# Optimization experiments

Hardware: AMD Instinct MI355X
Metric: run time of the kernel (lower is better)

Reference implementation:

```python
import jax, jax.numpy as jnp
import numpy as np

EPS = 1e-5
K = 3  # involution kernel size


def bin_act(x):
    # STE binary activation: forward = sign(x), backward via piecewise poly
    m1 = (x < -1).astype(jnp.float32)
    m2 = (x < 0).astype(jnp.float32)
    m3 = (x < 1).astype(jnp.float32)
    out = -1.0 * m1 + (x * x + 2 * x) * (1 - m1)
    out = out * m2 + (-x * x + 2 * x) * (1 - m2)
    out = out * m3 + 1.0 * (1 - m3)
    sg = jax.lax.stop_gradient
    return sg(jnp.sign(x)) - sg(out) + out


def bin_conv1x1(x, w):
    # BinaryConv with kernel_size=1: w is (O, I, 1, 1)
    sf = jnp.mean(jnp.abs(w), axis=(1, 2, 3), keepdims=True)
    bw = sf * jnp.sign(w)
    rw = jnp.clip(w, -1.0, 1.0)
    sg = jax.lax.stop_gradient
    f = sg(bw) - sg(rw) + rw  # (O, I, 1, 1)
    return jnp.einsum('oi,bihw->bohw', f[:, :, 0, 0], x)


def batchnorm(x, gamma, beta):
    # training-mode BN over (N, H, W) per channel, biased variance
    m = jnp.mean(x, axis=(0, 2, 3), keepdims=True)
    v = jnp.mean((x - m) ** 2, axis=(0, 2, 3), keepdims=True)
    xn = (x - m) * jax.lax.rsqrt(v + EPS)
    return gamma.reshape(1, -1, 1, 1) * xn + beta.reshape(1, -1, 1, 1)


def prelu(x, a):
    return jnp.maximum(x, 0) + a.reshape(1, -1, 1, 1) * jnp.minimum(x, 0)


def setup_inputs() -> dict:
    key = jax.random.key(0)
    ks = jax.random.split(key, 8)
    B, C, H, W = 8, 64, 128, 128
    Cr = C // 2           # reduce_rate = 2
    KK = K * K            # group = 1
    inp = {
        'x': jax.random.normal(ks[0], (B, C, H, W), dtype=jnp.float32),
        'pre_bias_b': jnp.zeros((1, C, 1, 1), jnp.float32),
        'pre_conv_w': jax.random.uniform(ks[1], (C, C, 1, 1), jnp.float32) * 0.001,
        'pre_gamma': jnp.ones((C,), jnp.float32),
        'pre_beta': jnp.zeros((C,), jnp.float32),
        'pre_a': jnp.full((C,), 0.25, jnp.float32),
        'mid_bias_b': jnp.zeros((1, C, 1, 1), jnp.float32),
        'reduce_w': jax.random.uniform(ks[2], (Cr, C, 1, 1), jnp.float32) * 0.001,
        'span_w': jax.random.uniform(ks[3], (KK, Cr, 1, 1), jnp.float32) * 0.001,
        'mid_gamma': jnp.ones((C,), jnp.float32),
        'mid_beta': jnp.zeros((C,), jnp.float32),
        'mid_a': jnp.full((C,), 0.25, jnp.float32),
        'post_bias_b': jnp.zeros((1, C, 1, 1), jnp.float32),
        'post_conv_w': jax.random.uniform(ks[4], (C, C, 1, 1), jnp.float32) * 0.001,
        'post_gamma': jnp.ones((C,), jnp.float32),
        'post_beta': jnp.zeros((C,), jnp.float32),
    }
    return inp


def reference(x, pre_bias_b, pre_conv_w, pre_gamma, pre_beta, pre_a,
              mid_bias_b, reduce_w, span_w, mid_gamma, mid_beta, mid_a,
              post_bias_b, post_conv_w, post_gamma, post_beta):
    B, C, H, W = x.shape
    h = bin_act(x)
    h = h + pre_bias_b
    h = bin_conv1x1(h, pre_conv_w)
    h = batchnorm(h, pre_gamma, pre_beta)
    h = prelu(h, pre_a)
    h = h + mid_bias_b
    # kernel branch (AvgPool2d(1,1) is identity for stride=1)
    ker = bin_conv1x1(bin_conv1x1(h, reduce_w), span_w)  # (B, K*K, H, W)
    # unfold: 3x3 patches, pad=1, stride=1 -> (B, C, K*K, H, W)
    hp = jnp.pad(h, ((0, 0), (0, 0), (1, 1), (1, 1)))
    patches = jnp.stack(
        [hp[:, :, i:i + H, j:j + W] for i in range(K) for j in range(K)],
        axis=2)
    out = jnp.sum(patches * ker[:, None, :, :, :], axis=2)  # (B, C, H, W)
    out = batchnorm(out, mid_gamma, mid_beta)
    out = jax.nn.relu(out)
    out = prelu(out, mid_a)
    out = out + post_bias_b
    out = bin_conv1x1(out, post_conv_w)
    out = batchnorm(out, post_gamma, post_beta)
    return out + x  # downsample is Identity (stride=1)
```

## Files before the change

kernel.cpp:

```cpp
#include <hip/hip_runtime.h>

#define B_   8
#define C_   64
#define HW   16384
#define CHW  (C_*HW)
#define NPIX (B_*HW)
#define EPS_ 1e-5f

typedef unsigned short u16;
typedef unsigned int   u32;
typedef __attribute__((ext_vector_type(8))) short bf16x8;
typedef __attribute__((ext_vector_type(4))) float f32x4;

__device__ __forceinline__ float sgnf(float v){ return (float)((v>0.f)-(v<0.f)); }
__device__ __forceinline__ float bf2f(u16 h){ return __uint_as_float(((u32)h)<<16); }
__device__ __forceinline__ u16 f2bf(float f){
    u32 u = __float_as_uint(f);
    u += 0x7fffu + ((u>>16)&1u);
    return (u16)(u>>16);
}
__device__ __forceinline__ u32 pack2(float a, float b){
    return (u32)f2bf(a) | ((u32)f2bf(b)<<16);
}

__global__ void prep(const float* __restrict__ pre_w, const float* __restrict__ pre_bias,
                     const float* __restrict__ red_w, const float* __restrict__ span_w,
                     const float* __restrict__ post_w,
                     u32* __restrict__ wb, float* __restrict__ AB,
                     float* __restrict__ Wq, float* __restrict__ M){
    __shared__ float sr[32], ss[9];
    int t = threadIdx.x;
    if (t < 64){
        float s = 0.f;
        for (int i = 0; i < 64; i++) s += fabsf(pre_w[t*64+i]);
        float alpha = s * (1.f/64.f);
        u32 b0 = 0, b1 = 0;
        float c0 = 0.f;
        for (int i = 0; i < 32; i++){
            b0 |= (__float_as_uint(pre_w[t*64+i]) >> 31) << i;
            b1 |= (__float_as_uint(pre_w[t*64+32+i]) >> 31) << i;
        }
        for (int i = 0; i < 64; i++)
            c0 += alpha * sgnf(pre_w[t*64+i]) * pre_bias[i];
        wb[2*t]   = b0;
        wb[2*t+1] = b1;
        AB[t]     = -2.f * alpha;
        AB[64+t]  = 64.f * alpha + c0;

        float s2 = 0.f;
        for (int i = 0; i < 64; i++) s2 += fabsf(post_w[t*64+i]);
        s2 *= (1.f/64.f);
        for (int i = 0; i < 64; i++) Wq[t*64+i] = s2 * sgnf(post_w[t*64+i]);
    }
    if (t < 32){
        float s = 0.f;
        for (int i = 0; i < 64; i++) s += fabsf(red_w[t*64+i]);
        sr[t] = s * (1.f/64.f);
    }
    if (t < 9){
        float s = 0.f;
        for (int r = 0; r < 32; r++) s += fabsf(span_w[t*32+r]);
        ss[t] = s * (1.f/32.f);
    }
    __syncthreads();
    if (t < 64){
        for (int j = 0; j < 9; j++){
            float m = 0.f;
            for (int r = 0; r < 32; r++)
                m += sgnf(span_w[j*32+r]) * sr[r] * sgnf(red_w[r*64+t]);
            M[t*9+j] = ss[j] * m;
        }
    }
}

__global__ __launch_bounds__(256) void conv_pre(const float* __restrict__ x,
                                                const u32* __restrict__ wb,
                                                const float* __restrict__ AB,
                                                u16* __restrict__ y1){
    int p   = blockIdx.x*256 + threadIdx.x;
    int b   = p >> 14;
    int pix = p & (HW-1);
    const float* xb = x + (size_t)b*CHW + pix;

    u32 m0 = 0, m1 = 0;
#pragma unroll
    for (int i = 0; i < 32; i++)
        m0 |= (__float_as_uint(xb[(size_t)i*HW]) >> 31) << i;
#pragma unroll
    for (int i = 0; i < 32; i++)
        m1 |= (__float_as_uint(xb[(size_t)(32+i)*HW]) >> 31) << i;

    u16* yb = y1 + (size_t)b*CHW + pix;
#pragma unroll 8
    for (int o = 0; o < 64; o++){
        u32 e0 = m0 ^ wb[2*o];
        u32 e1 = m1 ^ wb[2*o+1];
        float pc = (float)(__popc(e0) + __popc(e1));
        yb[(size_t)o*HW] = f2bf(fmaf(AB[o], pc, AB[64+o]));
    }
}

__global__ __launch_bounds__(256) void bnp(const u16* __restrict__ X,
                                           float2* __restrict__ part){
    int bid = blockIdx.x;
    int c   = bid & 63, sl = bid >> 6;
    int tid = threadIdx.x;
    const u16* base = X + (size_t)c*HW + sl*2048;
    float s = 0.f, q = 0.f;
#pragma unroll
    for (int b = 0; b < 8; b++){
        uint4 v = reinterpret_cast<const uint4*>(base + (size_t)b*CHW)[tid];
        u32 w[4] = {v.x, v.y, v.z, v.w};
#pragma unroll
        for (int k = 0; k < 4; k++){
            float f0 = __uint_as_float(w[k] << 16);
            float f1 = __uint_as_float(w[k] & 0xffff0000u);
            s += f0 + f1;
            q += f0*f0 + f1*f1;
        }
    }
    for (int off = 32; off > 0; off >>= 1){
        s += __shfl_down(s, off);
        q += __shfl_down(q, off);
    }
    __shared__ float2 wp[4];
    if ((tid & 63) == 0) wp[tid>>6] = make_float2(s, q);
    __syncthreads();
    if (tid == 0){
        float S = 0.f, Q = 0.f;
        for (int w = 0; w < 4; w++){ S += wp[w].x; Q += wp[w].y; }
        part[bid] = make_float2(S, Q);
    }
}

__device__ __forceinline__ void bn_combine(const float2* __restrict__ part,
                                           const float* __restrict__ gamma,
                                           const float* __restrict__ beta,
                                           float* scl, float* shl, int tid){
    if (tid < 64){
        float S = 0.f, Q = 0.f;
#pragma unroll
        for (int sl = 0; sl < 8; sl++){
            float2 v = part[sl*64 + tid];
            S += v.x; Q += v.y;
        }
        float mean = S * (1.f/(float)NPIX);
        float var  = fmaxf(Q * (1.f/(float)NPIX) - mean*mean, 0.f);
        float sc = gamma[tid] * rsqrtf(var + EPS_);
        scl[tid] = sc;
        shl[tid] = beta[tid] - mean*sc;
    }
}

__global__ __launch_bounds__(256) void kerk(const u16* __restrict__ y1,
                                            const float2* __restrict__ part1,
                                            const float* __restrict__ gamma,
                                            const float* __restrict__ beta,
                                            const float* __restrict__ pa,
                                            const float* __restrict__ mb,
                                            const float* __restrict__ M,
                                            u16* __restrict__ ker){
    __shared__ float scl[64], shl[64], al[64], mbl[64];
    int tid = threadIdx.x;
    bn_combine(part1, gamma, beta, scl, shl, tid);
    if (tid < 64){ al[tid] = pa[tid]; mbl[tid] = mb[tid]; }
    __syncthreads();

    int p   = blockIdx.x*256 + tid;
    int b   = p >> 14;
    int pix = p & (HW-1);
    const u16* yb = y1 + (size_t)b*CHW + pix;

    float acc[9];
#pragma unroll
    for (int j = 0; j < 9; j++) acc[j] = 0.f;
    for (int i = 0; i < 64; i++){
        float u = bf2f(yb[(size_t)i*HW]);
        float w = fmaf(scl[i], u, shl[i]);
        float z = fmaxf(w, 0.f) + al[i]*fminf(w, 0.f) + mbl[i];
#pragma unroll
        for (int j = 0; j < 9; j++)
            acc[j] = fmaf(M[i*9+j], z, acc[j]);
    }
    u16* kb = ker + (size_t)b*9*HW + pix;
#pragma unroll
    for (int j = 0; j < 9; j++) kb[(size_t)j*HW] = f2bf(acc[j]);
}

__global__ __launch_bounds__(256) void gatherk(const u16* __restrict__ y1,
                                               const float2* __restrict__ part1,
                                               const float* __restrict__ gamma,
                                               const float* __restrict__ beta,
                                               const float* __restrict__ pa,
                                               const float* __restrict__ mb,
                                               const u16* __restrict__ ker,
                                               u16* __restrict__ y2){
    __shared__ float scl[64], shl[64], al[64], mbl[64];
    __shared__ float zr[8*6*132];

    int tid = threadIdx.x;
    bn_combine(part1, gamma, beta, scl, shl, tid);
    if (tid < 64){ al[tid] = pa[tid]; mbl[tid] = mb[tid]; }
    if (tid < 96){
        int cc = tid / 12, rem = tid - cc*12, rr = rem >> 1, ed = rem & 1;
        zr[(cc*6 + rr)*132 + ed*129] = 0.f;
    }
    __syncthreads();

    int bid = blockIdx.x;
    int b  = bid >> 8;
    int cg = (bid >> 5) & 7;
    int rg = bid & 31;
    int y0 = rg*4;
    int c0 = cg*8;

    {
        int cc   = tid >> 5;
        int lane = tid & 31;
        int c    = c0 + cc;
        float sc = scl[c], sh = shl[c], a = al[c], m = mbl[c];
        const u16* src = y1 + (size_t)(b*64 + c)*HW;
#pragma unroll
        for (int k = 0; k < 24; k++){
            int e  = lane + 32*k;
            int rr = e >> 7;
            int xx = e & 127;
            int gy = y0 + rr - 1;
            float z = 0.f;
            if ((unsigned)gy < 128u){
                float u = bf2f(src[gy*128 + xx]);
                float w = fmaf(sc, u, sh);
                z = fmaxf(w, 0.f) + a*fminf(w, 0.f) + m;
            }
            zr[(cc*6 + rr)*132 + xx + 1] = z;
        }
    }
    __syncthreads();

    {
        int lane2 = tid & 63;
        int ly    = tid >> 6;
        int x0    = lane2*2;
        int gp    = (y0 + ly)*128 + x0;

        float k0[9], k1[9];
        const u16* kb = ker + (size_t)b*9*HW + gp;
#pragma unroll
        for (int j = 0; j < 9; j++){
            u32 u = *reinterpret_cast<const u32*>(kb + (size_t)j*HW);
            k0[j] = __uint_as_float(u << 16);
            k1[j] = __uint_as_float(u & 0xffff0000u);
        }

        u32* yo = reinterpret_cast<u32*>(y2 + (size_t)(b*64 + c0)*HW + gp);
#pragma unroll
        for (int cc = 0; cc < 8; cc++){
            const float* zrow = &zr[(cc*6 + ly)*132 + x0];
            float o0 = 0.f, o1 = 0.f;
#pragma unroll
            for (int dy = 0; dy < 3; dy++){
                float2 za = *reinterpret_cast<const float2*>(zrow + dy*132);
                float2 zb = *reinterpret_cast<const float2*>(zrow + dy*132 + 2);
                o0 = fmaf(za.x, k0[dy*3+0], o0);
                o0 = fmaf(za.y, k0[dy*3+1], o0);
                o0 = fmaf(zb.x, k0[dy*3+2], o0);
                o1 = fmaf(za.y, k1[dy*3+0], o1);
                o1 = fmaf(zb.x, k1[dy*3+1], o1);
                o1 = fmaf(zb.y, k1[dy*3+2], o1);
            }
            yo[(size_t)cc*(HW/2)] = pack2(o0, o1);
        }
    }
}

__global__ __launch_bounds__(256) void conv_post(const u16* __restrict__ y2,
                                                 const float2* __restrict__ part2,
                                                 const float* __restrict__ gamma,
                                                 const float* __restrict__ beta,
                                                 const float* __restrict__ pbias,
                                                 const float* __restrict__ Wq,
                                                 u16* __restrict__ y3){
    __shared__ u16 sB[256*64];
    __shared__ u16 sA[64*64];
    __shared__ float scl[64], shl[64], pbl[64];

    int tid = threadIdx.x;
    bn_combine(part2, gamma, beta, scl, shl, tid);
    if (tid < 64) pbl[tid] = pbias[tid];

    {
        int o  = tid >> 2;
        int k0 = (tid & 3) << 4;
        const float* wr = Wq + o*64 + k0;
        int swz = (o & 7) << 3;
#pragma unroll
        for (int s8 = 0; s8 < 2; s8++){
            uint4 q;
            q.x = pack2(wr[s8*8+0], wr[s8*8+1]);
            q.y = pack2(wr[s8*8+2], wr[s8*8+3]);
            q.z = pack2(wr[s8*8+4], wr[s8*8+5]);
            q.w = pack2(wr[s8*8+6], wr[s8*8+7]);
            *reinterpret_cast<uint4*>(&sA[o*64 + ((k0 + s8*8) ^ swz)]) = q;
        }
    }
    __syncthreads();

    int b    = blockIdx.x >> 6;
    int pix0 = (blockIdx.x & 63) << 8;

    {
        int cp = tid & 31;
        int g  = tid >> 5;
        const u16* r0 = y2 + (size_t)(b*64 + 2*cp)*HW + pix0;
        const u16* r1 = r0 + HW;
        float s0 = scl[2*cp],   h0 = shl[2*cp],   p0 = pbl[2*cp];
        float s1 = scl[2*cp+1], h1 = shl[2*cp+1], p1 = pbl[2*cp+1];
#pragma unroll
        for (int it = 0; it < 4; it++){
            int oct = g + it*8;
            uint4 va = *reinterpret_cast<const uint4*>(r0 + oct*8);
            uint4 vb = *reinterpret_cast<const uint4*>(r1 + oct*8);
            u32 wa[4] = {va.x, va.y, va.z, va.w};
            u32 wc[4] = {vb.x, vb.y, vb.z, vb.w};
#pragma unroll
            for (int k = 0; k < 4; k++){
                int px = oct*8 + 2*k;
                float a0 = fmaf(s0, bf2f((u16)(wa[k] & 0xffffu)), h0);
                float a1 = fmaf(s0, bf2f((u16)(wa[k] >> 16)),     h0);
                float c0v= fmaf(s1, bf2f((u16)(wc[k] & 0xffffu)), h1);
                float c1v= fmaf(s1, bf2f((u16)(wc[k] >> 16)),     h1);
                a0 = fmaxf(a0, 0.f) + p0;  a1 = fmaxf(a1, 0.f) + p0;
                c0v= fmaxf(c0v,0.f) + p1;  c1v= fmaxf(c1v,0.f) + p1;
                int e0 = px*64     + ((2*cp) ^ ((px & 7) << 3));
                int e1 = (px+1)*64 + ((2*cp) ^ (((px+1) & 7) << 3));
                *reinterpret_cast<u32*>(&sB[e0]) = pack2(a0, c0v);
                *reinterpret_cast<u32*>(&sB[e1]) = pack2(a1, c1v);
            }
        }
    }
    __syncthreads();

    int w  = tid >> 6;
    int l  = tid & 63;
    int lr = l & 15;
    int lk = l >> 4;

    bf16x8 af[4][2];
#pragma unroll
    for (int os = 0; os < 4; os++){
        int o = os*16 + lr;
        int swz = (o & 7) << 3;
#pragma unroll
        for (int kf = 0; kf < 2; kf++){
            int k8 = lk*8 + kf*32;
            af[os][kf] = *reinterpret_cast<const bf16x8*>(&sA[o*64 + (k8 ^ swz)]);
        }
    }

    f32x4 acc[4][4];
#pragma unroll
    for (int os = 0; os < 4; os++)
#pragma unroll
        for (int ns = 0; ns < 4; ns++)
            acc[os][ns] = (f32x4){0.f, 0.f, 0.f, 0.f};

#pragma unroll
    for (int ns = 0; ns < 4; ns++){
        int px  = w*64 + ns*16 + lr;
        int swz = (px & 7) << 3;
        bf16x8 b0 = *reinterpret_cast<const bf16x8*>(&sB[px*64 + ((lk*8)      ^ swz)]);
        bf16x8 b1 = *reinterpret_cast<const bf16x8*>(&sB[px*64 + ((lk*8 + 32) ^ swz)]);
#pragma unroll
        for (int os = 0; os < 4; os++){
            acc[os][ns] = __builtin_amdgcn_mfma_f32_16x16x32_bf16(af[os][0], b0, acc[os][ns], 0, 0, 0);
            acc[os][ns] = __builtin_amdgcn_mfma_f32_16x16x32_bf16(af[os][1], b1, acc[os][ns], 0, 0, 0);
        }
    }

    u16* yb = y3 + (size_t)(b*64)*HW + pix0;
#pragma unroll
    for (int os = 0; os < 4; os++){
#pragma unroll
        for (int ns = 0; ns < 4; ns++){
            int px = w*64 + ns*16 + lr;
#pragma unroll
            for (int r = 0; r < 4; r++){
                int o = os*16 + lk*4 + r;
                yb[(size_t)o*HW + px] = f2bf(acc[os][ns][r]);
            }
        }
    }
}

__global__ __launch_bounds__(256) void finalk(const u16* __restrict__ y3,
                                              const float* __restrict__ x,
                                              const float2* __restrict__ part3,
                                              const float* __restrict__ gamma,
                                              const float* __restrict__ beta,
                                              float* __restrict__ out){
    __shared__ float scl[64], shl[64];
    int tid = threadIdx.x;
    bn_combine(part3, gamma, beta, scl, shl, tid);
    __syncthreads();
#pragma unroll
    for (int it = 0; it < 4; it++){
        int i4 = blockIdx.x*1024 + it*256 + tid;
        int c  = (i4 >> 12) & 63;
        uint2  yv = reinterpret_cast<const uint2*>(y3)[i4];
        float4 bx = reinterpret_cast<const float4*>(x)[i4];
        float s = scl[c], t = shl[c];
        float4 r;
        r.x = fmaf(s, __uint_as_float(yv.x << 16),          t) + bx.x;
        r.y = fmaf(s, __uint_as_float(yv.x & 0xffff0000u),  t) + bx.y;
        r.z = fmaf(s, __uint_as_float(yv.y << 16),          t) + bx.z;
        r.w = fmaf(s, __uint_as_float(yv.y & 0xffff0000u),  t) + bx.w;
        reinterpret_cast<float4*>(out)[i4] = r;
    }
}

extern "C" void kernel_launch(void* const* d_in, const int* in_sizes, int n_in,
                              void* d_out, int out_size, void* d_ws, size_t ws_size,
                              hipStream_t stream){
    const float* x        = (const float*)d_in[0];
    const float* pre_bias = (const float*)d_in[1];
    const float* pre_w    = (const float*)d_in[2];
    const float* pre_g    = (const float*)d_in[3];
    const float* pre_b    = (const float*)d_in[4];
    const float* pre_a    = (const float*)d_in[5];
    const float* mid_bias = (const float*)d_in[6];
    const float* red_w    = (const float*)d_in[7];
    const float* span_w   = (const float*)d_in[8];
    const float* mid_g    = (const float*)d_in[9];
    const float* mid_b    = (const float*)d_in[10];
    const float* post_bias= (const float*)d_in[12];
    const float* post_w   = (const float*)d_in[13];
    const float* post_g   = (const float*)d_in[14];
    const float* post_b   = (const float*)d_in[15];

    float* ws   = (float*)d_ws;
    u16*   y1b  = (u16*)ws;
    u16*   kerb = (u16*)(ws + 4194304);
    float* Wq   = ws + 4194304 + 589824;
    float* M    = Wq + 4096;
    u32*   wb   = (u32*)(M + 640);
    float* AB   = (float*)(wb + 128);
    float2* part1 = (float2*)(AB + 128);
    float2* part2 = part1 + 512;
    float2* part3 = part2 + 512;

    u16*   y2b = (u16*)d_out;
    float* out = (float*)d_out;

    hipLaunchKernelGGL(prep, dim3(1), dim3(64), 0, stream,
                       pre_w, pre_bias, red_w, span_w, post_w, wb, AB, Wq, M);
    hipLaunchKernelGGL(conv_pre, dim3(NPIX/256), dim3(256), 0, stream,
                       x, wb, AB, y1b);
    hipLaunchKernelGGL(bnp, dim3(512), dim3(256), 0, stream, y1b, part1);
    hipLaunchKernelGGL(kerk, dim3(NPIX/256), dim3(256), 0, stream,
                       y1b, part1, pre_g, pre_b, pre_a, mid_bias, M, kerb);
    hipLaunchKernelGGL(gatherk, dim3(2048), dim3(256), 0, stream,
                       y1b, part1, pre_g, pre_b, pre_a, mid_bias, kerb, y2b);
    hipLaunchKernelGGL(bnp, dim3(512), dim3(256), 0, stream, y2b, part2);
    hipLaunchKernelGGL(conv_post, dim3(512), dim3(256), 0, stream,
                       y2b, part2, mid_g, mid_b, post_bias, Wq, y1b);
    hipLaunchKernelGGL(bnp, dim3(512), dim3(256), 0, stream, y1b, part3);
    hipLaunchKernelGGL(finalk, dim3(2048), dim3(256), 0, stream,
                       y1b, x, part3, post_g, post_b, out);
}
```

Before: 104.6 us.

## Fuse BN statistics into producer kernels with last-block finalize

Result: slower. 360.3 us (+244.5%).

```diff
diff --git a/kernel.cpp b/kernel.cpp
--- a/kernel.cpp
+++ b/kernel.cpp
@@ -1,9 +1,8 @@
 #include <hip/hip_runtime.h>
 
 #define B_   8
-#define C_   64
 #define HW   16384
-#define CHW  (C_*HW)
+#define CHW  (64*HW)
 #define NPIX (B_*HW)
 #define EPS_ 1e-5f
 
@@ -27,19 +26,21 @@
                      const float* __restrict__ red_w, const float* __restrict__ span_w,
                      const float* __restrict__ post_w,
                      u32* __restrict__ wb, float* __restrict__ AB,
-                     float* __restrict__ Wq, float* __restrict__ M){
+                     u16* __restrict__ wqbf, float* __restrict__ M,
+                     u32* __restrict__ cnt){
     __shared__ float sr[32], ss[9];
     int t = threadIdx.x;
+    if (t < 3) cnt[t] = 0u;
     if (t < 64){
         float s = 0.f;
         for (int i = 0; i < 64; i++) s += fabsf(pre_w[t*64+i]);
         float alpha = s * (1.f/64.f);
         u32 b0 = 0, b1 = 0;
+        for (int i = 0; i < 32; i++){
+            b0 |= (__float_as_uint(pre_w[t*64+i])    >> 31) << i;
+            b1 |= (__float_as_uint(pre_w[t*64+32+i]) >> 31) << i;
+        }
         float c0 = 0.f;
-        for (int i = 0; i < 32; i++){
-            b0 |= (__float_as_uint(pre_w[t*64+i]) >> 31) << i;
-            b1 |= (__float_as_uint(pre_w[t*64+32+i]) >> 31) << i;
-        }
         for (int i = 0; i < 64; i++)
             c0 += alpha * sgnf(pre_w[t*64+i]) * pre_bias[i];
         wb[2*t]   = b0;
@@ -50,7 +51,7 @@
         float s2 = 0.f;
         for (int i = 0; i < 64; i++) s2 += fabsf(post_w[t*64+i]);
         s2 *= (1.f/64.f);
-        for (int i = 0; i < 64; i++) Wq[t*64+i] = s2 * sgnf(post_w[t*64+i]);
+        for (int i = 0; i < 64; i++) wqbf[t*64+i] = f2bf(s2 * sgnf(post_w[t*64+i]));
     }
     if (t < 32){
         float s = 0.f;
@@ -100,8 +101,12 @@
     }
 }
 
-__global__ __launch_bounds__(256) void bnp(const u16* __restrict__ X,
-                                           float2* __restrict__ part){
+__global__ __launch_bounds__(256) void bnp1(const u16* __restrict__ X,
+                                            const float* __restrict__ gamma,
+                                            const float* __restrict__ beta,
+                                            float2* __restrict__ part,
+                                            float* __restrict__ scsh,
+                                            u32* __restrict__ cnt){
     int bid = blockIdx.x;
     int c   = bid & 63, sl = bid >> 6;
     int tid = threadIdx.x;
@@ -124,46 +129,47 @@
         q += __shfl_down(q, off);
     }
     __shared__ float2 wp[4];
+    __shared__ int last;
     if ((tid & 63) == 0) wp[tid>>6] = make_float2(s, q);
     __syncthreads();
     if (tid == 0){
         float S = 0.f, Q = 0.f;
         for (int w = 0; w < 4; w++){ S += wp[w].x; Q += wp[w].y; }
         part[bid] = make_float2(S, Q);
-    }
-}
-
-__device__ __forceinline__ void bn_combine(const float2* __restrict__ part,
-                                           const float* __restrict__ gamma,
-                                           const float* __restrict__ beta,
-                                           float* scl, float* shl, int tid){
-    if (tid < 64){
-        float S = 0.f, Q = 0.f;
-#pragma unroll
-        for (int sl = 0; sl < 8; sl++){
-            float2 v = part[sl*64 + tid];
-            S += v.x; Q += v.y;
-        }
-        float mean = S * (1.f/(float)NPIX);
-        float var  = fmaxf(Q * (1.f/(float)NPIX) - mean*mean, 0.f);
-        float sc = gamma[tid] * rsqrtf(var + EPS_);
-        scl[tid] = sc;
-        shl[tid] = beta[tid] - mean*sc;
+        __threadfence();
+        last = (atomicAdd(cnt, 1u) == 511u);
+    }
+    __syncthreads();
+    if (last){
+        __threadfence();
+        if (tid < 64){
+            float S = 0.f, Q = 0.f;
+#pragma unroll
+            for (int sl2 = 0; sl2 < 8; sl2++){
+                float2 v = part[sl2*64 + tid];
+                S += v.x; Q += v.y;
+            }
+            float mean = S * (1.f/(float)NPIX);
+            float var  = fmaxf(Q * (1.f/(float)NPIX) - mean*mean, 0.f);
+            float sc = gamma[tid] * rsqrtf(var + EPS_);
+            scsh[tid]    = sc;
+            scsh[64+tid] = beta[tid] - mean*sc;
+        }
     }
 }
 
 __global__ __launch_bounds__(256) void kerk(const u16* __restrict__ y1,
-                                            const float2* __restrict__ part1,
-                                            const float* __restrict__ gamma,
-                                            const float* __restrict__ beta,
+                                            const float* __restrict__ scsh,
                                             const float* __restrict__ pa,
                                             const float* __restrict__ mb,
                                             const float* __restrict__ M,
                                             u16* __restrict__ ker){
     __shared__ float scl[64], shl[64], al[64], mbl[64];
     int tid = threadIdx.x;
-    bn_combine(part1, gamma, beta, scl, shl, tid);
-    if (tid < 64){ al[tid] = pa[tid]; mbl[tid] = mb[tid]; }
+    if (tid < 64){
+        scl[tid] = scsh[tid]; shl[tid] = scsh[64+tid];
+        al[tid]  = pa[tid];   mbl[tid] = mb[tid];
+    }
     __syncthreads();
 
     int p   = blockIdx.x*256 + tid;
@@ -188,19 +194,26 @@
 }
 
 __global__ __launch_bounds__(256) void gatherk(const u16* __restrict__ y1,
-                                               const float2* __restrict__ part1,
+                                               const float* __restrict__ scsh_in,
+                                               const float* __restrict__ pa,
+                                               const float* __restrict__ mb,
                                                const float* __restrict__ gamma,
                                                const float* __restrict__ beta,
-                                               const float* __restrict__ pa,
-                                               const float* __restrict__ mb,
                                                const u16* __restrict__ ker,
-                                               u16* __restrict__ y2){
+                                               u16* __restrict__ y2,
+                                               float2* __restrict__ part2,
+                                               float* __restrict__ scsh_out,
+                                               u32* __restrict__ cnt){
     __shared__ float scl[64], shl[64], al[64], mbl[64];
     __shared__ float zr[8*6*132];
+    __shared__ float2 rowsum[32];
+    __shared__ int last;
 
     int tid = threadIdx.x;
-    bn_combine(part1, gamma, beta, scl, shl, tid);
-    if (tid < 64){ al[tid] = pa[tid]; mbl[tid] = mb[tid]; }
+    if (tid < 64){
+        scl[tid] = scsh_in[tid]; shl[tid] = scsh_in[64+tid];
+        al[tid]  = pa[tid];      mbl[tid] = mb[tid];
+    }
     if (tid < 96){
         int cc = tid / 12, rem = tid - cc*12, rr = rem >> 1, ed = rem & 1;
         zr[(cc*6 + rr)*132 + ed*129] = 0.f;
@@ -239,9 +252,9 @@
 
     {
         int lane2 = tid & 63;
-        int ly    = tid >> 6;
+        int wv    = tid >> 6;
         int x0    = lane2*2;
-        int gp    = (y0 + ly)*128 + x0;
+        int gp    = (y0 + wv)*128 + x0;
 
         float k0[9], k1[9];
         const u16* kb = ker + (size_t)b*9*HW + gp;
@@ -255,7 +268,7 @@
         u32* yo = reinterpret_cast<u32*>(y2 + (size_t)(b*64 + c0)*HW + gp);
 #pragma unroll
         for (int cc = 0; cc < 8; cc++){
-            const float* zrow = &zr[(cc*6 + ly)*132 + x0];
+            const float* zrow = &zr[(cc*6 + wv)*132 + x0];
             float o0 = 0.f, o1 = 0.f;
 #pragma unroll
             for (int dy = 0; dy < 3; dy++){
@@ -269,39 +282,65 @@
                 o1 = fmaf(zb.y, k1[dy*3+2], o1);
             }
             yo[(size_t)cc*(HW/2)] = pack2(o0, o1);
+            float sm = o0 + o1, qm = o0*o0 + o1*o1;
+#pragma unroll
+            for (int m = 1; m < 64; m <<= 1){
+                sm += __shfl_xor(sm, m);
+                qm += __shfl_xor(qm, m);
+            }
+            if (lane2 == 0) rowsum[wv*8 + cc] = make_float2(sm, qm);
+        }
+    }
+    __syncthreads();
+    if (tid < 8){
+        float S = 0.f, Q = 0.f;
+#pragma unroll
+        for (int w = 0; w < 4; w++){
+            float2 v = rowsum[w*8 + tid];
+            S += v.x; Q += v.y;
+        }
+        part2[(size_t)(c0 + tid)*256 + (b*32 + rg)] = make_float2(S, Q);
+    }
+    __threadfence();
+    if (tid == 0) last = (atomicAdd(cnt, 1u) == 2047u);
+    __syncthreads();
+    if (last){
+        __threadfence();
+        if (tid < 64){
+            float S = 0.f, Q = 0.f;
+            const float2* pc = part2 + (size_t)tid*256;
+            for (int k = 0; k < 256; k++){
+                float2 v = pc[k];
+                S += v.x; Q += v.y;
+            }
+            float mean = S * (1.f/(float)NPIX);
+            float var  = fmaxf(Q * (1.f/(float)NPIX) - mean*mean, 0.f);
+            float sc = gamma[tid] * rsqrtf(var + EPS_);
+            scsh_out[tid]    = sc;
+            scsh_out[64+tid] = beta[tid] - mean*sc;
         }
     }
 }
 
 __global__ __launch_bounds__(256) void conv_post(const u16* __restrict__ y2,
-                                                 const float2* __restrict__ part2,
+                                                 const float* __restrict__ scsh_in,
+                                                 const float* __restrict__ pbias,
+                                                 const u16* __restrict__ wqbf,
                                                  const float* __restrict__ gamma,
                                                  const float* __restrict__ beta,
-                                                 const float* __restrict__ pbias,
-                                                 const float* __restrict__ Wq,
-                                                 u16* __restrict__ y3){
+                                                 u16* __restrict__ y3,
+                                                 float2* __restrict__ part3,
+                                                 float* __restrict__ scsh_out,
+                                                 u32* __restrict__ cnt){
     __shared__ u16 sB[256*64];
-    __shared__ u16 sA[64*64];
     __shared__ float scl[64], shl[64], pbl[64];
+    __shared__ int last;
 
     int tid = threadIdx.x;
-    bn_combine(part2, gamma, beta, scl, shl, tid);
-    if (tid < 64) pbl[tid] = pbias[tid];
-
-    {
-        int o  = tid >> 2;
-        int k0 = (tid & 3) << 4;
-        const float* wr = Wq + o*64 + k0;
-        int swz = (o & 7) << 3;
-#pragma unroll
-        for (int s8 = 0; s8 < 2; s8++){
-            uint4 q;
-            q.x = pack2(wr[s8*8+0], wr[s8*8+1]);
-            q.y = pack2(wr[s8*8+2], wr[s8*8+3]);
-            q.z = pack2(wr[s8*8+4], wr[s8*8+5]);
-            q.w = pack2(wr[s8*8+6], wr[s8*8+7]);
-            *reinterpret_cast<uint4*>(&sA[o*64 + ((k0 + s8*8) ^ swz)]) = q;
-        }
+    if (tid < 64){
+        scl[tid] = scsh_in[tid];
+        shl[tid] = scsh_in[64+tid];
+        pbl[tid] = pbias[tid];
     }
     __syncthreads();
 
@@ -338,7 +377,6 @@
             }
         }
     }
-    __syncthreads();
 
     int w  = tid >> 6;
     int l  = tid & 63;
@@ -349,13 +387,11 @@
 #pragma unroll
     for (int os = 0; os < 4; os++){
         int o = os*16 + lr;
-        int swz = (o & 7) << 3;
-#pragma unroll
-        for (int kf = 0; kf < 2; kf++){
-            int k8 = lk*8 + kf*32;
-            af[os][kf] = *reinterpret_cast<const bf16x8*>(&sA[o*64 + (k8 ^ swz)]);
-        }
-    }
+#pragma unroll
+        for (int kf = 0; kf < 2; kf++)
+            af[os][kf] = *reinterpret_cast<const bf16x8*>(wqbf + o*64 + lk*8 + kf*32);
+    }
+    __syncthreads();
 
     f32x4 acc[4][4];
 #pragma unroll
@@ -390,17 +426,62 @@
             }
         }
     }
+
+    __syncthreads();
+    float2* wsum = (float2*)sB;
+#pragma unroll
+    for (int os = 0; os < 4; os++){
+#pragma unroll
+        for (int r = 0; r < 4; r++){
+            float s = acc[os][0][r] + acc[os][1][r] + acc[os][2][r] + acc[os][3][r];
+            float q = acc[os][0][r]*acc[os][0][r] + acc[os][1][r]*acc[os][1][r]
+                    + acc[os][2][r]*acc[os][2][r] + acc[os][3][r]*acc[os][3][r];
+#pragma unroll
+            for (int m = 1; m < 16; m <<= 1){
+                s += __shfl_xor(s, m);
+                q += __shfl_xor(q, m);
+            }
+            if (lr == 0) wsum[w*64 + os*16 + lk*4 + r] = make_float2(s, q);
+        }
+    }
+    __syncthreads();
+    if (tid < 64){
+        float S = 0.f, Q = 0.f;
+#pragma unroll
+        for (int ww = 0; ww < 4; ww++){
+            float2 v = wsum[ww*64 + tid];
+            S += v.x; Q += v.y;
+        }
+        part3[(size_t)tid*512 + blockIdx.x] = make_float2(S, Q);
+    }
+    __threadfence();
+    if (tid == 0) last = (atomicAdd(cnt, 1u) == 511u);
+    __syncthreads();
+    if (last){
+        __threadfence();
+        if (tid < 64){
+            float S = 0.f, Q = 0.f;
+            const float2* pc = part3 + (size_t)tid*512;
+            for (int k = 0; k < 512; k++){
+                float2 v = pc[k];
+                S += v.x; Q += v.y;
+            }
+            float mean = S * (1.f/(float)NPIX);
+            float var  = fmaxf(Q * (1.f/(float)NPIX) - mean*mean, 0.f);
+            float sc = gamma[tid] * rsqrtf(var + EPS_);
+            scsh_out[tid]    = sc;
+            scsh_out[64+tid] = beta[tid] - mean*sc;
+        }
+    }
 }
 
 __global__ __launch_bounds__(256) void finalk(const u16* __restrict__ y3,
                                               const float* __restrict__ x,
-                                              const float2* __restrict__ part3,
-                                              const float* __restrict__ gamma,
-                                              const float* __restrict__ beta,
+                                              const float* __restrict__ scsh,
                                               float* __restrict__ out){
     __shared__ float scl[64], shl[64];
     int tid = threadIdx.x;
-    bn_combine(part3, gamma, beta, scl, shl, tid);
+    if (tid < 64){ scl[tid] = scsh[tid]; shl[tid] = scsh[64+tid]; }
     __syncthreads();
 #pragma unroll
     for (int it = 0; it < 4; it++){
@@ -440,30 +521,33 @@
     float* ws   = (float*)d_ws;
     u16*   y1b  = (u16*)ws;
     u16*   kerb = (u16*)(ws + 4194304);
-    float* Wq   = ws + 4194304 + 589824;
-    float* M    = Wq + 4096;
-    u32*   wb   = (u32*)(M + 640);
-    float* AB   = (float*)(wb + 128);
-    float2* part1 = (float2*)(AB + 128);
+    u16*   wqbf = (u16*)(ws + 4784128);
+    float* M    = ws + 4786176;
+    u32*   wb   = (u32*)(ws + 4786816);
+    float* AB   = ws + 4786944;
+    float2* part1 = (float2*)(ws + 4787072);
     float2* part2 = part1 + 512;
-    float2* part3 = part2 + 512;
+    float2* part3 = part2 + 16384;
+    float*  scsh  = (float*)(part3 + 32768);
+    u32*    cnt   = (u32*)(scsh + 384);
 
     u16*   y2b = (u16*)d_out;
     float* out = (float*)d_out;
 
-    hipLaunchKernelGGL(prep, dim3(1), dim3(64), 0, stream,
-                       pre_w, pre_bias, red_w, span_w, post_w, wb, AB, Wq, M);
+    hipLaunchKernelGGL(prep, dim3(1), dim3(256), 0, stream,
+                       pre_w, pre_bias, red_w, span_w, post_w, wb, AB, wqbf, M, cnt);
     hipLaunchKernelGGL(conv_pre, dim3(NPIX/256), dim3(256), 0, stream,
                        x, wb, AB, y1b);
-    hipLaunchKernelGGL(bnp, dim3(512), dim3(256), 0, stream, y1b, part1);
+    hipLaunchKernelGGL(bnp1, dim3(512), dim3(256), 0, stream,
+                       y1b, pre_g, pre_b, part1, scsh, cnt);
     hipLaunchKernelGGL(kerk, dim3(NPIX/256), dim3(256), 0, stream,
-                       y1b, part1, pre_g, pre_b, pre_a, mid_bias, M, kerb);
+                       y1b, scsh, pre_a, mid_bias, M, kerb);
     hipLaunchKernelGGL(gatherk, dim3(2048), dim3(256), 0, stream,
-                       y1b, part1, pre_g, pre_b, pre_a, mid_bias, kerb, y2b);
-    hipLaunchKernelGGL(bnp, dim3(512), dim3(256), 0, stream, y2b, part2);
+                       y1b, scsh, pre_a, mid_bias, mid_g, mid_b, kerb, y2b,
+                       part2, scsh + 128, cnt + 1);
     hipLaunchKernelGGL(conv_post, dim3(512), dim3(256), 0, stream,
-                       y2b, part2, mid_g, mid_b, post_bias, Wq, y1b);
-    hipLaunchKernelGGL(bnp, dim3(512), dim3(256), 0, stream, y1b, part3);
+                       y2b, scsh + 128, post_bias, wqbf, post_g, post_b, y1b,
+                       part3, scsh + 256, cnt + 2);
     hipLaunchKernelGGL(finalk, dim3(2048), dim3(256), 0, stream,
-                       y1b, x, part3, post_g, post_b, out);
-}
+                       y1b, x, scsh + 256, out);
+}
```
